# Kernel tuning notes

Hardware: AMD Instinct MI355X
Metric: run time of the kernel (lower is better)

Reference implementation:

```python
import jax, jax.numpy as jnp
import numpy as np
import math

N_NODES = 100000
N_EDGES = 1600000
DIM = 64

def setup_inputs() -> dict:
    key = jax.random.key(0)
    k_x, k_w, k_w1, k_row, k_col, k_dd = jax.random.split(key, 6)
    stdv = 1.0 / math.sqrt(DIM)
    X = jax.random.normal(k_x, (N_NODES, DIM), dtype=jnp.float32)
    W = jax.random.uniform(k_w, (DIM, DIM), dtype=jnp.float32, minval=-stdv, maxval=stdv)
    W1 = jax.random.uniform(k_w1, (DIM, DIM), dtype=jnp.float32, minval=-stdv, maxval=stdv)
    # CSR expansion of the graph: row_ids sorted (destination node of each edge)
    row_ids = jnp.sort(jax.random.randint(k_row, (N_EDGES,), 0, N_NODES, dtype=jnp.int32))
    col_ids = jax.random.randint(k_col, (N_EDGES,), 0, N_NODES, dtype=jnp.int32)
    # degree-like positive normalization vector, bounded away from 0
    dd1 = jax.random.uniform(k_dd, (N_NODES, 1), dtype=jnp.float32, minval=0.5, maxval=1.5)
    return {"X": X, "W": W, "W1": W1, "dd1": dd1, "row_ids": row_ids, "col_ids": col_ids}

def reference(X, W, W1, dd1, row_ids, col_ids):
    # X_prime = X @ W  (dense GEMM)
    XW = X @ W  # [N, D]
    # SpMM aggregation: out[i] = sum_{j in neighbors(i)} XW[j]
    agg = jax.ops.segment_sum(XW[col_ids], row_ids, num_segments=X.shape[0])  # [N, D]
    # per-node normalization + residual branch X @ W1
    return agg / dd1 + X @ W1
```

## Files before the change

### kernel.cpp

```cpp
#include <hip/hip_runtime.h>
#include <hip/hip_bf16.h>

#define DIMS 64

__global__ __launch_bounds__(256) void gcn_gemm2(
    const float* __restrict__ X, const float* __restrict__ W,
    const float* __restrict__ W1, __hip_bfloat16* __restrict__ XWh,
    float* __restrict__ out, int N)
{
    __shared__ float Ws[64 * 64];
    __shared__ float W1s[64 * 64];
    __shared__ float Xs[64 * 68];

    const int t = threadIdx.x;

    for (int i = t; i < 1024; i += 256) {
        reinterpret_cast<float4*>(Ws)[i]  = reinterpret_cast<const float4*>(W)[i];
        reinterpret_cast<float4*>(W1s)[i] = reinterpret_cast<const float4*>(W1)[i];
    }

    const int row0 = blockIdx.x * 64;

    for (int i = t; i < 1024; i += 256) {
        const int r  = i >> 4;
        const int k4 = (i & 15) * 4;
        const int row = row0 + r;
        float4 v = make_float4(0.f, 0.f, 0.f, 0.f);
        if (row < N)
            v = reinterpret_cast<const float4*>(X)[(size_t)row * 16 + (i & 15)];
        Xs[(k4 + 0) * 68 + r] = v.x;
        Xs[(k4 + 1) * 68 + r] = v.y;
        Xs[(k4 + 2) * 68 + r] = v.z;
        Xs[(k4 + 3) * 68 + r] = v.w;
    }
    __syncthreads();

    const int dg = t & 15;
    const int rg = t >> 4;

    float4 acc[4];
    float4 acc1[4];
    #pragma unroll
    for (int r = 0; r < 4; ++r) {
        acc[r]  = make_float4(0.f, 0.f, 0.f, 0.f);
        acc1[r] = make_float4(0.f, 0.f, 0.f, 0.f);
    }

    #pragma unroll 4
    for (int k = 0; k < 64; ++k) {
        const float4 x4 = *reinterpret_cast<const float4*>(&Xs[k * 68 + rg * 4]);
        const float4 w  = *reinterpret_cast<const float4*>(&Ws[k * 64 + dg * 4]);
        const float4 w1 = *reinterpret_cast<const float4*>(&W1s[k * 64 + dg * 4]);
        const float xr[4] = {x4.x, x4.y, x4.z, x4.w};
        #pragma unroll
        for (int r = 0; r < 4; ++r) {
            acc[r].x  += xr[r] * w.x;  acc[r].y  += xr[r] * w.y;
            acc[r].z  += xr[r] * w.z;  acc[r].w  += xr[r] * w.w;
            acc1[r].x += xr[r] * w1.x; acc1[r].y += xr[r] * w1.y;
            acc1[r].z += xr[r] * w1.z; acc1[r].w += xr[r] * w1.w;
        }
    }

    #pragma unroll
    for (int r = 0; r < 4; ++r) {
        const int row = row0 + rg * 4 + r;
        if (row < N) {
            reinterpret_cast<float4*>(out)[(size_t)row * 16 + dg] = acc1[r];
            uint2 pk;
            __hip_bfloat16* ph = reinterpret_cast<__hip_bfloat16*>(&pk);
            ph[0] = __float2bfloat16(acc[r].x);
            ph[1] = __float2bfloat16(acc[r].y);
            ph[2] = __float2bfloat16(acc[r].z);
            ph[3] = __float2bfloat16(acc[r].w);
            reinterpret_cast<uint2*>(XWh)[(size_t)row * 16 + dg] = pk;
        }
    }
}

__global__ __launch_bounds__(256) void build_row_ptr(
    const int* __restrict__ rows, int* __restrict__ ptr,
    __hip_bfloat16* __restrict__ XWh, int E, int N)
{
    const int e = blockIdx.x * 256 + threadIdx.x;
    if (blockIdx.x == 0 && threadIdx.x < 32)
        reinterpret_cast<uint32_t*>(XWh + (size_t)N * DIMS)[threadIdx.x] = 0u;
    if (e >= E) return;
    const int r1 = rows[e];
    const int r0 = (e == 0) ? -1 : rows[e - 1];
    for (int r = r0 + 1; r <= r1; ++r) ptr[r] = e;
    if (e == E - 1) {
        for (int r = r1 + 1; r <= N; ++r) ptr[r] = E;
    }
}

#define BATCH 8

__global__ __launch_bounds__(256) void gcn_csr(
    const __hip_bfloat16* __restrict__ XWh, const float* __restrict__ dd1,
    const int* __restrict__ ptr, const int* __restrict__ cols,
    float* __restrict__ out, int N, int E)
{
    const int t    = blockIdx.x * 256 + threadIdx.x;
    const int wave = t >> 6;
    const int lane = threadIdx.x & 63;
    const int g    = lane >> 3;
    const int d    = lane & 7;

    const int row = wave * 8 + g;
    int p0 = 0, p1 = 0;
    if (row < N) { p0 = ptr[row]; p1 = ptr[row + 1]; }

    float2 acc[4];
    #pragma unroll
    for (int k = 0; k < 4; ++k) acc[k] = make_float2(0.f, 0.f);

    for (int e = p0; __any(e < p1); e += BATCH) {
        uint4 raw[BATCH];
        #pragma unroll
        for (int j = 0; j < BATCH; ++j) {
            const int ee = e + j;
            const int es = (ee < E) ? ee : (E - 1);
            const int cl = cols[es];
            const int c  = (ee < p1) ? cl : N;
            raw[j] = *reinterpret_cast<const uint4*>(
                XWh + (((size_t)c) << 6) + (d << 3));
        }
        #pragma unroll
        for (int j = 0; j < BATCH; ++j) {
            const uint32_t w0 = raw[j].x, w1 = raw[j].y, w2 = raw[j].z, w3 = raw[j].w;
            acc[0].x += __uint_as_float(w0 << 16);
            acc[0].y += __uint_as_float(w0 & 0xffff0000u);
            acc[1].x += __uint_as_float(w1 << 16);
            acc[1].y += __uint_as_float(w1 & 0xffff0000u);
            acc[2].x += __uint_as_float(w2 << 16);
            acc[2].y += __uint_as_float(w2 & 0xffff0000u);
            acc[3].x += __uint_as_float(w3 << 16);
            acc[3].y += __uint_as_float(w3 & 0xffff0000u);
        }
    }

    if (row < N) {
        const float s = 1.0f / dd1[row];
        float4* po = reinterpret_cast<float4*>(out + (size_t)row * DIMS + d * 8);
        float4 o0 = po[0];
        float4 o1 = po[1];
        o0.x += acc[0].x * s;  o0.y += acc[0].y * s;
        o0.z += acc[1].x * s;  o0.w += acc[1].y * s;
        o1.x += acc[2].x * s;  o1.y += acc[2].y * s;
        o1.z += acc[3].x * s;  o1.w += acc[3].y * s;
        po[0] = o0;
        po[1] = o1;
    }
}

extern "C" void kernel_launch(void* const* d_in, const int* in_sizes, int n_in,
                              void* d_out, int out_size, void* d_ws, size_t ws_size,
                              hipStream_t stream) {
    const float* X   = (const float*)d_in[0];
    const float* W   = (const float*)d_in[1];
    const float* W1  = (const float*)d_in[2];
    const float* dd1 = (const float*)d_in[3];
    const int* rows  = (const int*)d_in[4];
    const int* cols  = (const int*)d_in[5];

    const int N = in_sizes[3];
    const int E = in_sizes[4];

    char* wsp = (char*)d_ws;
    __hip_bfloat16* XWh = (__hip_bfloat16*)wsp;
    size_t off = (((size_t)(N + 1) * DIMS * sizeof(__hip_bfloat16)) + 255) & ~(size_t)255;
    int* row_ptr = (int*)(wsp + off);

    float* out = (float*)d_out;

    hipLaunchKernelGGL(build_row_ptr, dim3((E + 255) / 256), dim3(256), 0, stream,
                       rows, row_ptr, XWh, E, N);

    hipLaunchKernelGGL(gcn_gemm2, dim3((N + 63) / 64), dim3(256), 0, stream,
                       X, W, W1, XWh, out, N);

    const int waves  = (N + 7) / 8;
    const int blocks = (waves + 3) / 4;
    hipLaunchKernelGGL(gcn_csr, dim3(blocks), dim3(256), 0, stream,
                       XWh, dd1, row_ptr, cols, out, N, E);
}
```

Baseline: 145.7 us.

## Split XW table into four feature chunks for cache-resident CSR gather

```diff
diff --git a/kernel.cpp b/kernel.cpp
--- a/kernel.cpp
+++ b/kernel.cpp
@@ -2,10 +2,12 @@
 #include <hip/hip_bf16.h>
 
 #define DIMS 64
+#define BATCH 8
+#define NCHUNK 4
 
 __global__ __launch_bounds__(256) void gcn_gemm2(
     const float* __restrict__ X, const float* __restrict__ W,
-    const float* __restrict__ W1, __hip_bfloat16* __restrict__ XWh,
+    const float* __restrict__ W1, __hip_bfloat16* __restrict__ XWc,
     float* __restrict__ out, int N)
 {
     __shared__ float Ws[64 * 64];
@@ -61,6 +63,8 @@
         }
     }
 
+    const int c    = dg >> 2;
+    const int slot = dg & 3;
     #pragma unroll
     for (int r = 0; r < 4; ++r) {
         const int row = row0 + rg * 4 + r;
@@ -72,18 +76,21 @@
             ph[1] = __float2bfloat16(acc[r].y);
             ph[2] = __float2bfloat16(acc[r].z);
             ph[3] = __float2bfloat16(acc[r].w);
-            reinterpret_cast<uint2*>(XWh)[(size_t)row * 16 + dg] = pk;
+            reinterpret_cast<uint2*>(XWc)[((size_t)c * (N + 1) + row) * 4 + slot] = pk;
         }
     }
 }
 
 __global__ __launch_bounds__(256) void build_row_ptr(
     const int* __restrict__ rows, int* __restrict__ ptr,
-    __hip_bfloat16* __restrict__ XWh, int E, int N)
+    __hip_bfloat16* __restrict__ XWc, int E, int N)
 {
     const int e = blockIdx.x * 256 + threadIdx.x;
-    if (blockIdx.x == 0 && threadIdx.x < 32)
-        reinterpret_cast<uint32_t*>(XWh + (size_t)N * DIMS)[threadIdx.x] = 0u;
+    if (blockIdx.x == 0 && threadIdx.x < 32) {
+        const int c = threadIdx.x >> 3;
+        const int w = threadIdx.x & 7;
+        reinterpret_cast<uint32_t*>(XWc)[((size_t)c * (N + 1) + N) * 8 + w] = 0u;
+    }
     if (e >= E) return;
     const int r1 = rows[e];
     const int r0 = (e == 0) ? -1 : rows[e - 1];
@@ -93,26 +100,27 @@
     }
 }
 
-#define BATCH 8
-
 __global__ __launch_bounds__(256) void gcn_csr(
-    const __hip_bfloat16* __restrict__ XWh, const float* __restrict__ dd1,
+    const __hip_bfloat16* __restrict__ XWc, const float* __restrict__ dd1,
     const int* __restrict__ ptr, const int* __restrict__ cols,
     float* __restrict__ out, int N, int E)
 {
-    const int t    = blockIdx.x * 256 + threadIdx.x;
-    const int wave = t >> 6;
-    const int lane = threadIdx.x & 63;
-    const int g    = lane >> 3;
-    const int d    = lane & 7;
+    const int chunk = blockIdx.x & 3;
+    const int rblk  = blockIdx.x >> 2;
+    const int wv    = threadIdx.x >> 6;
+    const int lane  = threadIdx.x & 63;
+    const int r     = lane >> 1;
+    const int h     = lane & 1;
 
-    const int row = wave * 8 + g;
+    const int row = (rblk * 4 + wv) * 32 + r;
     int p0 = 0, p1 = 0;
     if (row < N) { p0 = ptr[row]; p1 = ptr[row + 1]; }
 
-    float2 acc[4];
+    const __hip_bfloat16* tbl = XWc + ((size_t)chunk * (N + 1)) * 16;
+
+    float acc[8];
     #pragma unroll
-    for (int k = 0; k < 4; ++k) acc[k] = make_float2(0.f, 0.f);
+    for (int k = 0; k < 8; ++k) acc[k] = 0.f;
 
     for (int e = p0; __any(e < p1); e += BATCH) {
         uint4 raw[BATCH];
@@ -123,31 +131,32 @@
             const int cl = cols[es];
             const int c  = (ee < p1) ? cl : N;
             raw[j] = *reinterpret_cast<const uint4*>(
-                XWh + (((size_t)c) << 6) + (d << 3));
+                reinterpret_cast<const char*>(tbl) + (size_t)c * 32 + h * 16);
         }
         #pragma unroll
         for (int j = 0; j < BATCH; ++j) {
             const uint32_t w0 = raw[j].x, w1 = raw[j].y, w2 = raw[j].z, w3 = raw[j].w;
-            acc[0].x += __uint_as_float(w0 << 16);
-            acc[0].y += __uint_as_float(w0 & 0xffff0000u);
-            acc[1].x += __uint_as_float(w1 << 16);
-            acc[1].y += __uint_as_float(w1 & 0xffff0000u);
-            acc[2].x += __uint_as_float(w2 << 16);
-            acc[2].y += __uint_as_float(w2 & 0xffff0000u);
-            acc[3].x += __uint_as_float(w3 << 16);
-            acc[3].y += __uint_as_float(w3 & 0xffff0000u);
+            acc[0] += __uint_as_float(w0 << 16);
+            acc[1] += __uint_as_float(w0 & 0xffff0000u);
+            acc[2] += __uint_as_float(w1 << 16);
+            acc[3] += __uint_as_float(w1 & 0xffff0000u);
+            acc[4] += __uint_as_float(w2 << 16);
+            acc[5] += __uint_as_float(w2 & 0xffff0000u);
+            acc[6] += __uint_as_float(w3 << 16);
+            acc[7] += __uint_as_float(w3 & 0xffff0000u);
         }
     }
 
     if (row < N) {
         const float s = 1.0f / dd1[row];
-        float4* po = reinterpret_cast<float4*>(out + (size_t)row * DIMS + d * 8);
+        float4* po = reinterpret_cast<float4*>(
+            out + (size_t)row * DIMS + chunk * 16 + h * 8);
         float4 o0 = po[0];
         float4 o1 = po[1];
-        o0.x += acc[0].x * s;  o0.y += acc[0].y * s;
-        o0.z += acc[1].x * s;  o0.w += acc[1].y * s;
-        o1.x += acc[2].x * s;  o1.y += acc[2].y * s;
-        o1.z += acc[3].x * s;  o1.w += acc[3].y * s;
+        o0.x += acc[0] * s;  o0.y += acc[1] * s;
+        o0.z += acc[2] * s;  o0.w += acc[3] * s;
+        o1.x += acc[4] * s;  o1.y += acc[5] * s;
+        o1.z += acc[6] * s;  o1.w += acc[7] * s;
         po[0] = o0;
         po[1] = o1;
     }
@@ -167,20 +176,19 @@
     const int E = in_sizes[4];
 
     char* wsp = (char*)d_ws;
-    __hip_bfloat16* XWh = (__hip_bfloat16*)wsp;
-    size_t off = (((size_t)(N + 1) * DIMS * sizeof(__hip_bfloat16)) + 255) & ~(size_t)255;
+    __hip_bfloat16* XWc = (__hip_bfloat16*)wsp;
+    size_t off = (((size_t)NCHUNK * (N + 1) * 16 * sizeof(__hip_bfloat16)) + 255) & ~(size_t)255;
     int* row_ptr = (int*)(wsp + off);
 
     float* out = (float*)d_out;
 
     hipLaunchKernelGGL(build_row_ptr, dim3((E + 255) / 256), dim3(256), 0, stream,
-                       rows, row_ptr, XWh, E, N);
+                       rows, row_ptr, XWc, E, N);
 
     hipLaunchKernelGGL(gcn_gemm2, dim3((N + 63) / 64), dim3(256), 0, stream,
-                       X, W, W1, XWh, out, N);
+                       X, W, W1, XWc, out, N);
 
-    const int waves  = (N + 7) / 8;
-    const int blocks = (waves + 3) / 4;
-    hipLaunchKernelGGL(gcn_csr, dim3(blocks), dim3(256), 0, stream,
-                       XWh, dd1, row_ptr, cols, out, N, E);
+    const int rblks  = (N + 127) / 128;
+    hipLaunchKernelGGL(gcn_csr, dim3(rblks * NCHUNK), dim3(256), 0, stream,
+                       XWc, dd1, row_ptr, cols, out, N, E);
 }
```

Measured after the change: 173.8 us. +19.3%, slower.

## Use bf16 MFMA for dual GEMM and store residual in bf16 workspace

Applied to the files above, without the earlier changes.

```diff
diff --git a/kernel.cpp b/kernel.cpp
--- a/kernel.cpp
+++ b/kernel.cpp
@@ -2,77 +2,82 @@
 #include <hip/hip_bf16.h>
 
 #define DIMS 64
-
-__global__ __launch_bounds__(256) void gcn_gemm2(
+#define BATCH 8
+
+typedef short  bf16x8 __attribute__((ext_vector_type(8)));
+typedef float  f32x4v __attribute__((ext_vector_type(4)));
+
+static __device__ __forceinline__ short f2bf(float f) {
+    __hip_bfloat16 h = __float2bfloat16(f);
+    return *reinterpret_cast<short*>(&h);
+}
+
+__global__ __launch_bounds__(256) void gcn_gemm_mfma(
     const float* __restrict__ X, const float* __restrict__ W,
     const float* __restrict__ W1, __hip_bfloat16* __restrict__ XWh,
-    float* __restrict__ out, int N)
+    __hip_bfloat16* __restrict__ XW1h, int N)
 {
-    __shared__ float Ws[64 * 64];
-    __shared__ float W1s[64 * 64];
-    __shared__ float Xs[64 * 68];
-
-    const int t = threadIdx.x;
-
-    for (int i = t; i < 1024; i += 256) {
-        reinterpret_cast<float4*>(Ws)[i]  = reinterpret_cast<const float4*>(W)[i];
-        reinterpret_cast<float4*>(W1s)[i] = reinterpret_cast<const float4*>(W1)[i];
-    }
-
-    const int row0 = blockIdx.x * 64;
-
-    for (int i = t; i < 1024; i += 256) {
-        const int r  = i >> 4;
-        const int k4 = (i & 15) * 4;
-        const int row = row0 + r;
-        float4 v = make_float4(0.f, 0.f, 0.f, 0.f);
-        if (row < N)
-            v = reinterpret_cast<const float4*>(X)[(size_t)row * 16 + (i & 15)];
-        Xs[(k4 + 0) * 68 + r] = v.x;
-        Xs[(k4 + 1) * 68 + r] = v.y;
-        Xs[(k4 + 2) * 68 + r] = v.z;
-        Xs[(k4 + 3) * 68 + r] = v.w;
-    }
-    __syncthreads();
-
-    const int dg = t & 15;
-    const int rg = t >> 4;
-
-    float4 acc[4];
-    float4 acc1[4];
+    const int w    = threadIdx.x >> 6;
+    const int lane = threadIdx.x & 63;
+    const int L    = lane & 15;
+    const int q    = lane >> 4;
+
+    const int row0 = blockIdx.x * 64 + w * 16;
+    const int rowA = row0 + L;
+    const int rowC = (rowA < N) ? rowA : (N - 1);
+
+    bf16x8 bfrag[2][2][4];
+    #pragma unroll
+    for (int kh = 0; kh < 2; ++kh)
+        #pragma unroll
+        for (int nt = 0; nt < 4; ++nt)
+            #pragma unroll
+            for (int j = 0; j < 8; ++j) {
+                const int k = kh * 32 + q * 8 + j;
+                bfrag[0][kh][nt][j] = f2bf(W [k * 64 + nt * 16 + L]);
+                bfrag[1][kh][nt][j] = f2bf(W1[k * 64 + nt * 16 + L]);
+            }
+
+    f32x4v acc[2][4];
+    #pragma unroll
+    for (int m = 0; m < 2; ++m)
+        #pragma unroll
+        for (int nt = 0; nt < 4; ++nt)
+            acc[m][nt] = (f32x4v){0.f, 0.f, 0.f, 0.f};
+
+    #pragma unroll
+    for (int kh = 0; kh < 2; ++kh) {
+        const float4 xa = reinterpret_cast<const float4*>(
+            X + (size_t)rowC * 64 + kh * 32 + q * 8)[0];
+        const float4 xb = reinterpret_cast<const float4*>(
+            X + (size_t)rowC * 64 + kh * 32 + q * 8)[1];
+        bf16x8 a;
+        a[0] = f2bf(xa.x); a[1] = f2bf(xa.y); a[2] = f2bf(xa.z); a[3] = f2bf(xa.w);
+        a[4] = f2bf(xb.x); a[5] = f2bf(xb.y); a[6] = f2bf(xb.z); a[7] = f2bf(xb.w);
+        #pragma unroll
+        for (int nt = 0; nt < 4; ++nt) {
+            acc[0][nt] = __builtin_amdgcn_mfma_f32_16x16x32_bf16(
+                a, bfrag[0][kh][nt], acc[0][nt], 0, 0, 0);
+            acc[1][nt] = __builtin_amdgcn_mfma_f32_16x16x32_bf16(
+                a, bfrag[1][kh][nt], acc[1][nt], 0, 0, 0);
+        }
+    }
+
     #pragma unroll
     for (int r = 0; r < 4; ++r) {
-        acc[r]  = make_float4(0.f, 0.f, 0.f, 0.f);
-        acc1[r] = make_float4(0.f, 0.f, 0.f, 0.f);
-    }
-
-    #pragma unroll 4
-    for (int k = 0; k < 64; ++k) {
-        const float4 x4 = *reinterpret_cast<const float4*>(&Xs[k * 68 + rg * 4]);
-        const float4 w  = *reinterpret_cast<const float4*>(&Ws[k * 64 + dg * 4]);
-        const float4 w1 = *reinterpret_cast<const float4*>(&W1s[k * 64 + dg * 4]);
-        const float xr[4] = {x4.x, x4.y, x4.z, x4.w};
-        #pragma unroll
-        for (int r = 0; r < 4; ++r) {
-            acc[r].x  += xr[r] * w.x;  acc[r].y  += xr[r] * w.y;
-            acc[r].z  += xr[r] * w.z;  acc[r].w  += xr[r] * w.w;
-            acc1[r].x += xr[r] * w1.x; acc1[r].y += xr[r] * w1.y;
-            acc1[r].z += xr[r] * w1.z; acc1[r].w += xr[r] * w1.w;
-        }
-    }
-
-    #pragma unroll
-    for (int r = 0; r < 4; ++r) {
-        const int row = row0 + rg * 4 + r;
+        const int row = row0 + q * 4 + r;
         if (row < N) {
-            reinterpret_cast<float4*>(out)[(size_t)row * 16 + dg] = acc1[r];
-            uint2 pk;
-            __hip_bfloat16* ph = reinterpret_cast<__hip_bfloat16*>(&pk);
-            ph[0] = __float2bfloat16(acc[r].x);
-            ph[1] = __float2bfloat16(acc[r].y);
-            ph[2] = __float2bfloat16(acc[r].z);
-            ph[3] = __float2bfloat16(acc[r].w);
-            reinterpret_cast<uint2*>(XWh)[(size_t)row * 16 + dg] = pk;
+            ushort4 p0, p1;
+            p0.x = (unsigned short)f2bf(acc[0][0][r]);
+            p0.y = (unsigned short)f2bf(acc[0][1][r]);
+            p0.z = (unsigned short)f2bf(acc[0][2][r]);
+            p0.w = (unsigned short)f2bf(acc[0][3][r]);
+            p1.x = (unsigned short)f2bf(acc[1][0][r]);
+            p1.y = (unsigned short)f2bf(acc[1][1][r]);
+            p1.z = (unsigned short)f2bf(acc[1][2][r]);
+            p1.w = (unsigned short)f2bf(acc[1][3][r]);
+            *reinterpret_cast<ushort4*>(XWh  + ((size_t)row << 6) + 4 * L) = p0;
+            *reinterpret_cast<ushort4*>(XW1h + ((size_t)row << 6) + 4 * L) = p1;
         }
     }
 }
@@ -83,7 +88,7 @@
 {
     const int e = blockIdx.x * 256 + threadIdx.x;
     if (blockIdx.x == 0 && threadIdx.x < 32)
-        reinterpret_cast<uint32_t*>(XWh + (size_t)N * DIMS)[threadIdx.x] = 0u;
+        reinterpret_cast<uint32_t*>(XWh + ((size_t)N << 6))[threadIdx.x] = 0u;
     if (e >= E) return;
     const int r1 = rows[e];
     const int r0 = (e == 0) ? -1 : rows[e - 1];
@@ -93,12 +98,10 @@
     }
 }
 
-#define BATCH 8
-
 __global__ __launch_bounds__(256) void gcn_csr(
-    const __hip_bfloat16* __restrict__ XWh, const float* __restrict__ dd1,
-    const int* __restrict__ ptr, const int* __restrict__ cols,
-    float* __restrict__ out, int N, int E)
+    const __hip_bfloat16* __restrict__ XWh, const __hip_bfloat16* __restrict__ XW1h,
+    const float* __restrict__ dd1, const int* __restrict__ ptr,
+    const int* __restrict__ cols, float* __restrict__ out, int N, int E)
 {
     const int t    = blockIdx.x * 256 + threadIdx.x;
     const int wave = t >> 6;
@@ -110,9 +113,9 @@
     int p0 = 0, p1 = 0;
     if (row < N) { p0 = ptr[row]; p1 = ptr[row + 1]; }
 
-    float2 acc[4];
-    #pragma unroll
-    for (int k = 0; k < 4; ++k) acc[k] = make_float2(0.f, 0.f);
+    float acc[8];
+    #pragma unroll
+    for (int k = 0; k < 8; ++k) acc[k] = 0.f;
 
     for (int e = p0; __any(e < p1); e += BATCH) {
         uint4 raw[BATCH];
@@ -128,28 +131,38 @@
         #pragma unroll
         for (int j = 0; j < BATCH; ++j) {
             const uint32_t w0 = raw[j].x, w1 = raw[j].y, w2 = raw[j].z, w3 = raw[j].w;
-            acc[0].x += __uint_as_float(w0 << 16);
-            acc[0].y += __uint_as_float(w0 & 0xffff0000u);
-            acc[1].x += __uint_as_float(w1 << 16);
-            acc[1].y += __uint_as_float(w1 & 0xffff0000u);
-            acc[2].x += __uint_as_float(w2 << 16);
-            acc[2].y += __uint_as_float(w2 & 0xffff0000u);
-            acc[3].x += __uint_as_float(w3 << 16);
-            acc[3].y += __uint_as_float(w3 & 0xffff0000u);
+            acc[0] += __uint_as_float(w0 << 16);
+            acc[1] += __uint_as_float(w0 & 0xffff0000u);
+            acc[2] += __uint_as_float(w1 << 16);
+            acc[3] += __uint_as_float(w1 & 0xffff0000u);
+            acc[4] += __uint_as_float(w2 << 16);
+            acc[5] += __uint_as_float(w2 & 0xffff0000u);
+            acc[6] += __uint_as_float(w3 << 16);
+            acc[7] += __uint_as_float(w3 & 0xffff0000u);
         }
     }
 
     if (row < N) {
         const float s = 1.0f / dd1[row];
-        float4* po = reinterpret_cast<float4*>(out + (size_t)row * DIMS + d * 8);
-        float4 o0 = po[0];
-        float4 o1 = po[1];
-        o0.x += acc[0].x * s;  o0.y += acc[0].y * s;
-        o0.z += acc[1].x * s;  o0.w += acc[1].y * s;
-        o1.x += acc[2].x * s;  o1.y += acc[2].y * s;
-        o1.z += acc[3].x * s;  o1.w += acc[3].y * s;
-        po[0] = o0;
-        po[1] = o1;
+        const uint4 rr = *reinterpret_cast<const uint4*>(
+            XW1h + (((size_t)row) << 6) + (d << 3));
+        float res[8];
+        res[0] = __uint_as_float(rr.x << 16);
+        res[1] = __uint_as_float(rr.x & 0xffff0000u);
+        res[2] = __uint_as_float(rr.y << 16);
+        res[3] = __uint_as_float(rr.y & 0xffff0000u);
+        res[4] = __uint_as_float(rr.z << 16);
+        res[5] = __uint_as_float(rr.z & 0xffff0000u);
+        res[6] = __uint_as_float(rr.w << 16);
+        res[7] = __uint_as_float(rr.w & 0xffff0000u);
+        #pragma unroll
+        for (int tt = 0; tt < 4; ++tt) {
+            float2 o;
+            o.x = acc[tt]     * s + res[tt];
+            o.y = acc[4 + tt] * s + res[4 + tt];
+            *reinterpret_cast<float2*>(
+                out + ((size_t)row << 6) + tt * 16 + d * 2) = o;
+        }
     }
 }
 
@@ -169,6 +182,8 @@
     char* wsp = (char*)d_ws;
     __hip_bfloat16* XWh = (__hip_bfloat16*)wsp;
     size_t off = (((size_t)(N + 1) * DIMS * sizeof(__hip_bfloat16)) + 255) & ~(size_t)255;
+    __hip_bfloat16* XW1h = (__hip_bfloat16*)(wsp + off);
+    off += (((size_t)N * DIMS * sizeof(__hip_bfloat16)) + 255) & ~(size_t)255;
     int* row_ptr = (int*)(wsp + off);
 
     float* out = (float*)d_out;
@@ -176,11 +191,11 @@
     hipLaunchKernelGGL(build_row_ptr, dim3((E + 255) / 256), dim3(256), 0, stream,
                        rows, row_ptr, XWh, E, N);
 
-    hipLaunchKernelGGL(gcn_gemm2, dim3((N + 63) / 64), dim3(256), 0, stream,
-                       X, W, W1, XWh, out, N);
+    hipLaunchKernelGGL(gcn_gemm_mfma, dim3((N + 63) / 64), dim3(256), 0, stream,
+                       X, W, W1, XWh, XW1h, N);
 
     const int waves  = (N + 7) / 8;
     const int blocks = (waves + 3) / 4;
     hipLaunchKernelGGL(gcn_csr, dim3(blocks), dim3(256), 0, stream,
-                       XWh, dd1, row_ptr, cols, out, N, E);
-}
+                       XWh, XW1h, dd1, row_ptr, cols, out, N, E);
+}
```

Measured after the change: 135.9 us. 1.07x faster.
